# Kernel tuning notes

Measured on AMD Instinct MI355X. Metric: run time of the kernel, lower is better.

Reference implementation:

```python
import jax, jax.numpy as jnp
import numpy as np

N_NODES = 100000
N_EDGES = 1600000
D_IN = 128
D_OUT = 128
DROP_P = 0.5


def setup_inputs() -> dict:
    key = jax.random.key(0)
    k1, k2, k3, k4, k5, k6 = jax.random.split(key, 6)
    x = jax.random.normal(k1, (N_NODES, D_IN), dtype=jnp.float32)
    # xavier_normal init for w
    std = (2.0 / (D_IN + D_OUT)) ** 0.5
    w = jax.random.normal(k2, (D_IN, D_OUT), dtype=jnp.float32) * std
    b = jax.random.normal(k3, (D_OUT,), dtype=jnp.float32) * 0.01
    edge_row = jax.random.randint(k4, (N_EDGES,), 0, N_NODES, dtype=jnp.int32)
    edge_col = jax.random.randint(k5, (N_EDGES,), 0, N_NODES, dtype=jnp.int32)
    # normalized adjacency weights (e.g. 1/sqrt(d_i d_j)); use uniform positives
    edge_val = jax.random.uniform(k6, (N_EDGES,), dtype=jnp.float32)
    # dropout mask: keep with prob (1-p), scaled by 1/(1-p)
    km = jax.random.fold_in(key, 7)
    keep = jax.random.uniform(km, (N_NODES, D_IN)) >= DROP_P
    dropout_mask = keep.astype(jnp.float32) / (1.0 - DROP_P)
    return {"x": x, "w": w, "b": b, "edge_row": edge_row,
            "edge_col": edge_col, "edge_val": edge_val,
            "dropout_mask": dropout_mask}


def reference(x, w, b, edge_row, edge_col, edge_val, dropout_mask):
    # dropout (training mode) -> dense mm -> spmm(adj, xw) -> +b -> relu
    h = (x * dropout_mask) @ w                      # [N, D_OUT]
    msgs = h[edge_col] * edge_val[:, None]          # gather src feats, scale [E, D_OUT]
    agg = jax.ops.segment_sum(msgs, edge_row, num_segments=N_NODES)  # scatter-add to dst
    return jax.nn.relu(agg + b)
```

## Files before the change

### kernel.cpp

```cpp
#include <hip/hip_runtime.h>

#define N_NODES 100000
#define N_EDGES 1600000
#define D 128
#define MAXDEG 48

#define GEMM_NB ((N_NODES + 63) / 64)
#define HIST_NB (N_EDGES / 256)
#define TOTAL_NB (GEMM_NB + HIST_NB)

typedef __attribute__((ext_vector_type(8))) short short8;
typedef __attribute__((ext_vector_type(4))) short short4v;
typedef __attribute__((ext_vector_type(4))) float floatx4;
typedef __attribute__((ext_vector_type(2))) float floatx2;

__device__ __forceinline__ short f2bf(float f) {
    unsigned u = __float_as_uint(f);
    u += 0x7FFFu + ((u >> 16) & 1u);
    return (short)(u >> 16);
}

#define LDSK 136
__global__ __launch_bounds__(256) void gemm_hist_fill(const float* __restrict__ x,
                                                      const float* __restrict__ mask,
                                                      const float* __restrict__ w,
                                                      unsigned short* __restrict__ h,
                                                      const int* __restrict__ erow,
                                                      const int* __restrict__ ecol,
                                                      const float* __restrict__ eval,
                                                      int* __restrict__ deg,
                                                      unsigned long long* __restrict__ pairs) {
    const unsigned bid = blockIdx.x;
    const int t = threadIdx.x;

    if (bid % 5 != 0) {
        const int hi = (int)(bid - bid / 5 - 1);
        const int e = hi * 256 + t;
        const int r = erow[e];
        const int k = atomicAdd(&deg[r], 1);
        if (k < MAXDEG) {
            const unsigned long long pv =
                (unsigned long long)(unsigned)ecol[e] |
                ((unsigned long long)(unsigned)__float_as_uint(eval[e]) << 32);
            pairs[(size_t)r * MAXDEG + k] = pv;
        }
        return;
    }
    const int gb = (int)(bid / 5);

    __shared__ short w_s[128 * LDSK];
#pragma unroll
    for (int i = 0; i < 4; ++i) {
        const int id = t + 256 * i;
        const int n0 = (id & 31) * 4;
        const int k0 = (id >> 5) * 4;
        short tr[4][4];
#pragma unroll
        for (int r = 0; r < 4; ++r) {
            const float4 wv = *(const float4*)(w + (size_t)(k0 + r) * D + n0);
            tr[r][0] = f2bf(wv.x); tr[r][1] = f2bf(wv.y);
            tr[r][2] = f2bf(wv.z); tr[r][3] = f2bf(wv.w);
        }
#pragma unroll
        for (int c = 0; c < 4; ++c) {
            short4v v = {tr[0][c], tr[1][c], tr[2][c], tr[3][c]};
            *(short4v*)(&w_s[(n0 + c) * LDSK + k0]) = v;
        }
    }
    __syncthreads();

    const int wave = t >> 6, lane = t & 63;
    const int m = lane & 15, quad = lane >> 4;
    const int r0w = gb * 64 + wave * 16;
    int arow = r0w + m;
    if (arow >= N_NODES) arow = N_NODES - 1;
    const floatx4* xp4 = (const floatx4*)(x + (size_t)arow * D);
    const floatx4* mp4 = (const floatx4*)(mask + (size_t)arow * D);

    floatx4 acc[8];
#pragma unroll
    for (int tt = 0; tt < 8; ++tt) acc[tt] = (floatx4){0.f, 0.f, 0.f, 0.f};

#pragma unroll
    for (int kc = 0; kc < 4; ++kc) {
        const int kb = kc * 32 + quad * 8;
        const floatx4 xa = __builtin_nontemporal_load(xp4 + kb / 4);
        const floatx4 xb = __builtin_nontemporal_load(xp4 + kb / 4 + 1);
        const floatx4 ma = __builtin_nontemporal_load(mp4 + kb / 4);
        const floatx4 mb = __builtin_nontemporal_load(mp4 + kb / 4 + 1);
        short8 a;
#pragma unroll
        for (int j = 0; j < 4; ++j) a[j] = f2bf(xa[j] * ma[j]);
#pragma unroll
        for (int j = 0; j < 4; ++j) a[4 + j] = f2bf(xb[j] * mb[j]);
#pragma unroll
        for (int tt = 0; tt < 8; ++tt) {
            const short8 bfrag = *(const short8*)(&w_s[(tt * 16 + m) * LDSK + kb]);
            acc[tt] = __builtin_amdgcn_mfma_f32_16x16x32_bf16(a, bfrag, acc[tt], 0, 0, 0);
        }
    }

    __syncthreads();
    short* ep = w_s + wave * 16 * LDSK;
#pragma unroll
    for (int tt = 0; tt < 8; ++tt) {
        const int col = tt * 16 + m;
#pragma unroll
        for (int i = 0; i < 4; ++i)
            ep[(quad * 4 + i) * LDSK + col] = f2bf(acc[tt][i]);
    }
    __syncthreads();

    const int rrow = lane >> 2;
    const int chunk = lane & 3;
    const int gr = r0w + rrow;
    if (gr < N_NODES) {
        const short* src = ep + rrow * LDSK + chunk * 32;
        unsigned short* dst = h + (size_t)gr * D + chunk * 32;
#pragma unroll
        for (int j = 0; j < 4; ++j)
            *(short8*)(dst + j * 8) = *(const short8*)(src + j * 8);
    }
}

__global__ __launch_bounds__(256) void gather_kernel(const unsigned* __restrict__ h2,
                                                     const int* __restrict__ deg,
                                                     const unsigned long long* __restrict__ pairs,
                                                     const float* __restrict__ b,
                                                     float* __restrict__ out) {
    const int lane = threadIdx.x & 63;
    const int rA = blockIdx.x * 8 + (threadIdx.x >> 6) * 2;
    const int rB = rA + 1;

    int dgA = deg[rA]; if (dgA > MAXDEG) dgA = MAXDEG;
    int dgB = deg[rB]; if (dgB > MAXDEG) dgB = MAXDEG;

    const int pl = (lane < MAXDEG) ? lane : (MAXDEG - 1);
    const unsigned long long pvA = pairs[(size_t)rA * MAXDEG + pl];
    const unsigned long long pvB = pairs[(size_t)rB * MAXDEG + pl];
    const unsigned cAv = (unsigned)pvA;
    const unsigned wAv = (unsigned)(pvA >> 32);
    const unsigned cBv = (unsigned)pvB;
    const unsigned wBv = (unsigned)(pvB >> 32);

    float axA = 0.f, ayA = 0.f, axB = 0.f, ayB = 0.f;
    const int mx = (dgA > dgB) ? dgA : dgB;

    for (int b0 = 0; b0 < mx; b0 += 8) {
        unsigned uA[8], uB[8];
        float vA[8], vB[8];
#pragma unroll
        for (int jj = 0; jj < 8; ++jj) {
            const int j = b0 + jj;
            const unsigned colA = (j < dgA)
                ? (unsigned)__builtin_amdgcn_readlane((int)cAv, j) : 0u;
            vA[jj] = (j < dgA)
                ? __uint_as_float((unsigned)__builtin_amdgcn_readlane((int)wAv, j)) : 0.f;
            uA[jj] = h2[(size_t)colA * 64 + lane];
            const unsigned colB = (j < dgB)
                ? (unsigned)__builtin_amdgcn_readlane((int)cBv, j) : 0u;
            vB[jj] = (j < dgB)
                ? __uint_as_float((unsigned)__builtin_amdgcn_readlane((int)wBv, j)) : 0.f;
            uB[jj] = h2[(size_t)colB * 64 + lane];
        }
#pragma unroll
        for (int jj = 0; jj < 8; ++jj) {
            axA += __uint_as_float(uA[jj] << 16) * vA[jj];
            ayA += __uint_as_float(uA[jj] & 0xFFFF0000u) * vA[jj];
            axB += __uint_as_float(uB[jj] << 16) * vB[jj];
            ayB += __uint_as_float(uB[jj] & 0xFFFF0000u) * vB[jj];
        }
    }

    const float2 bv = ((const float2*)b)[lane];
    floatx2 oA, oB;
    oA.x = fmaxf(axA + bv.x, 0.f);
    oA.y = fmaxf(ayA + bv.y, 0.f);
    oB.x = fmaxf(axB + bv.x, 0.f);
    oB.y = fmaxf(ayB + bv.y, 0.f);
    __builtin_nontemporal_store(oA, (floatx2*)(out + (size_t)rA * D) + lane);
    __builtin_nontemporal_store(oB, (floatx2*)(out + (size_t)rB * D) + lane);
}

extern "C" void kernel_launch(void* const* d_in, const int* in_sizes, int n_in,
                              void* d_out, int out_size, void* d_ws, size_t ws_size,
                              hipStream_t stream) {
    const float* x    = (const float*)d_in[0];
    const float* w    = (const float*)d_in[1];
    const float* b    = (const float*)d_in[2];
    const int*   erow = (const int*)d_in[3];
    const int*   ecol = (const int*)d_in[4];
    const float* eval = (const float*)d_in[5];
    const float* mask = (const float*)d_in[6];
    float* out = (float*)d_out;

    char* base = (char*)d_ws;
    unsigned short* h = (unsigned short*)(base);
    int* deg          = (int*)(base + 25600000);
    unsigned long long* pairs = (unsigned long long*)(base + 26000000);

    (void)hipMemsetAsync(deg, 0, N_NODES * sizeof(int), stream);

    gemm_hist_fill<<<TOTAL_NB, 256, 0, stream>>>(x, mask, w, h, erow, ecol, eval, deg, pairs);
    gather_kernel<<<N_NODES / 8, 256, 0, stream>>>((const unsigned*)h, deg, pairs, b, out);
}
```

Measured before the change: 278.5 us.

## Amortize W staging over four GEMM tiles, write h directly, deepen gather batching

GEMM blocks now each process four 64-row tiles, so the bf16 transpose of W into LDS is paid once per four tiles, and the interleave ratio with histogram blocks changes from 1:4 to 1:16. The MFMA operands are swapped so each lane holds four consecutive output columns, which lets results go straight to global memory as short4 stores and removes the LDS epilogue and its barriers. The x and mask loads drop their nontemporal hint. In the gather kernel, sixteen rows per batch are fetched before accumulating, and the weight readlanes move into the accumulate loop, raising memory-level parallelism at the cost of more registers.

```diff
diff --git a/kernel.cpp b/kernel.cpp
--- a/kernel.cpp
+++ b/kernel.cpp
@@ -5,8 +5,10 @@
 #define D 128
 #define MAXDEG 48
 
-#define GEMM_NB ((N_NODES + 63) / 64)
+#define TILES_PER_GB 4
+#define GEMM_NB 391
 #define HIST_NB (N_EDGES / 256)
+#define RATIO 17
 #define TOTAL_NB (GEMM_NB + HIST_NB)
 
 typedef __attribute__((ext_vector_type(8))) short short8;
@@ -33,8 +35,8 @@
     const unsigned bid = blockIdx.x;
     const int t = threadIdx.x;
 
-    if (bid % 5 != 0) {
-        const int hi = (int)(bid - bid / 5 - 1);
+    if (bid % RATIO != 0) {
+        const int hi = (int)(bid - bid / RATIO - 1);
         const int e = hi * 256 + t;
         const int r = erow[e];
         const int k = atomicAdd(&deg[r], 1);
@@ -46,7 +48,7 @@
         }
         return;
     }
-    const int gb = (int)(bid / 5);
+    const int gb = (int)(bid / RATIO);
 
     __shared__ short w_s[128 * LDSK];
 #pragma unroll
@@ -71,55 +73,47 @@
 
     const int wave = t >> 6, lane = t & 63;
     const int m = lane & 15, quad = lane >> 4;
-    const int r0w = gb * 64 + wave * 16;
-    int arow = r0w + m;
-    if (arow >= N_NODES) arow = N_NODES - 1;
-    const floatx4* xp4 = (const floatx4*)(x + (size_t)arow * D);
-    const floatx4* mp4 = (const floatx4*)(mask + (size_t)arow * D);
-
-    floatx4 acc[8];
-#pragma unroll
-    for (int tt = 0; tt < 8; ++tt) acc[tt] = (floatx4){0.f, 0.f, 0.f, 0.f};
-
-#pragma unroll
-    for (int kc = 0; kc < 4; ++kc) {
-        const int kb = kc * 32 + quad * 8;
-        const floatx4 xa = __builtin_nontemporal_load(xp4 + kb / 4);
-        const floatx4 xb = __builtin_nontemporal_load(xp4 + kb / 4 + 1);
-        const floatx4 ma = __builtin_nontemporal_load(mp4 + kb / 4);
-        const floatx4 mb = __builtin_nontemporal_load(mp4 + kb / 4 + 1);
-        short8 a;
-#pragma unroll
-        for (int j = 0; j < 4; ++j) a[j] = f2bf(xa[j] * ma[j]);
-#pragma unroll
-        for (int j = 0; j < 4; ++j) a[4 + j] = f2bf(xb[j] * mb[j]);
-#pragma unroll
-        for (int tt = 0; tt < 8; ++tt) {
-            const short8 bfrag = *(const short8*)(&w_s[(tt * 16 + m) * LDSK + kb]);
-            acc[tt] = __builtin_amdgcn_mfma_f32_16x16x32_bf16(a, bfrag, acc[tt], 0, 0, 0);
-        }
-    }
-
-    __syncthreads();
-    short* ep = w_s + wave * 16 * LDSK;
-#pragma unroll
-    for (int tt = 0; tt < 8; ++tt) {
-        const int col = tt * 16 + m;
-#pragma unroll
-        for (int i = 0; i < 4; ++i)
-            ep[(quad * 4 + i) * LDSK + col] = f2bf(acc[tt][i]);
-    }
-    __syncthreads();
-
-    const int rrow = lane >> 2;
-    const int chunk = lane & 3;
-    const int gr = r0w + rrow;
-    if (gr < N_NODES) {
-        const short* src = ep + rrow * LDSK + chunk * 32;
-        unsigned short* dst = h + (size_t)gr * D + chunk * 32;
-#pragma unroll
-        for (int j = 0; j < 4; ++j)
-            *(short8*)(dst + j * 8) = *(const short8*)(src + j * 8);
+
+    for (int tile = 0; tile < TILES_PER_GB; ++tile) {
+        const int r0w = (gb * TILES_PER_GB + tile) * 64 + wave * 16;
+        if (r0w >= N_NODES) break;
+        int arow = r0w + m;
+        if (arow >= N_NODES) arow = N_NODES - 1;
+        const floatx4* xp4 = (const floatx4*)(x + (size_t)arow * D);
+        const floatx4* mp4 = (const floatx4*)(mask + (size_t)arow * D);
+
+        floatx4 acc[8];
+#pragma unroll
+        for (int tt = 0; tt < 8; ++tt) acc[tt] = (floatx4){0.f, 0.f, 0.f, 0.f};
+
+#pragma unroll
+        for (int kc = 0; kc < 4; ++kc) {
+            const int kb = kc * 32 + quad * 8;
+            const floatx4 xa = xp4[kb / 4];
+            const floatx4 xb = xp4[kb / 4 + 1];
+            const floatx4 ma = mp4[kb / 4];
+            const floatx4 mb = mp4[kb / 4 + 1];
+            short8 a;
+#pragma unroll
+            for (int j = 0; j < 4; ++j) a[j] = f2bf(xa[j] * ma[j]);
+#pragma unroll
+            for (int j = 0; j < 4; ++j) a[4 + j] = f2bf(xb[j] * mb[j]);
+#pragma unroll
+            for (int tt = 0; tt < 8; ++tt) {
+                const short8 wfrag = *(const short8*)(&w_s[(tt * 16 + m) * LDSK + kb]);
+                acc[tt] = __builtin_amdgcn_mfma_f32_16x16x32_bf16(wfrag, a, acc[tt], 0, 0, 0);
+            }
+        }
+
+        if (r0w + m < N_NODES) {
+            unsigned short* hp = h + (size_t)(r0w + m) * D + quad * 4;
+#pragma unroll
+            for (int tt = 0; tt < 8; ++tt) {
+                short4v hv = {f2bf(acc[tt][0]), f2bf(acc[tt][1]),
+                              f2bf(acc[tt][2]), f2bf(acc[tt][3])};
+                *(short4v*)(hp + tt * 16) = hv;
+            }
+        }
     }
 }
 
@@ -146,29 +140,29 @@
     float axA = 0.f, ayA = 0.f, axB = 0.f, ayB = 0.f;
     const int mx = (dgA > dgB) ? dgA : dgB;
 
-    for (int b0 = 0; b0 < mx; b0 += 8) {
-        unsigned uA[8], uB[8];
-        float vA[8], vB[8];
-#pragma unroll
-        for (int jj = 0; jj < 8; ++jj) {
+    for (int b0 = 0; b0 < mx; b0 += 16) {
+        unsigned uA[16], uB[16];
+#pragma unroll
+        for (int jj = 0; jj < 16; ++jj) {
             const int j = b0 + jj;
             const unsigned colA = (j < dgA)
                 ? (unsigned)__builtin_amdgcn_readlane((int)cAv, j) : 0u;
-            vA[jj] = (j < dgA)
-                ? __uint_as_float((unsigned)__builtin_amdgcn_readlane((int)wAv, j)) : 0.f;
             uA[jj] = h2[(size_t)colA * 64 + lane];
             const unsigned colB = (j < dgB)
                 ? (unsigned)__builtin_amdgcn_readlane((int)cBv, j) : 0u;
-            vB[jj] = (j < dgB)
+            uB[jj] = h2[(size_t)colB * 64 + lane];
+        }
+#pragma unroll
+        for (int jj = 0; jj < 16; ++jj) {
+            const int j = b0 + jj;
+            const float vA = (j < dgA)
+                ? __uint_as_float((unsigned)__builtin_amdgcn_readlane((int)wAv, j)) : 0.f;
+            const float vB = (j < dgB)
                 ? __uint_as_float((unsigned)__builtin_amdgcn_readlane((int)wBv, j)) : 0.f;
-            uB[jj] = h2[(size_t)colB * 64 + lane];
-        }
-#pragma unroll
-        for (int jj = 0; jj < 8; ++jj) {
-            axA += __uint_as_float(uA[jj] << 16) * vA[jj];
-            ayA += __uint_as_float(uA[jj] & 0xFFFF0000u) * vA[jj];
-            axB += __uint_as_float(uB[jj] << 16) * vB[jj];
-            ayB += __uint_as_float(uB[jj] & 0xFFFF0000u) * vB[jj];
+            axA += __uint_as_float(uA[jj] << 16) * vA;
+            ayA += __uint_as_float(uA[jj] & 0xFFFF0000u) * vA;
+            axB += __uint_as_float(uB[jj] << 16) * vB;
+            ayB += __uint_as_float(uB[jj] & 0xFFFF0000u) * vB;
         }
     }
 
```

Result: slower. 308.3 us (+10.7%).

## Process two 64-row tiles per GEMM block with register prefetch of inputs

Applied to the files above, without the earlier changes.

Each GEMM block now handles 128 rows in two 64-row passes. This amortizes the bf16 transpose of W into LDS over twice as many rows and halves the GEMM block count. The x and mask loads for the first tile are issued before the W staging, and the second tile's loads are issued before the first tile's epilogue, to overlap global latency with compute. It also gives the epilogue its own LDS buffer, removing the barriers, and changes the hist/GEMM block interleave ratio to 9. The cost is more registers and LDS per block, which may lower occupancy.

```diff
diff --git a/kernel.cpp b/kernel.cpp
--- a/kernel.cpp
+++ b/kernel.cpp
@@ -5,7 +5,7 @@
 #define D 128
 #define MAXDEG 48
 
-#define GEMM_NB ((N_NODES + 63) / 64)
+#define GEMM_NB 782
 #define HIST_NB (N_EDGES / 256)
 #define TOTAL_NB (GEMM_NB + HIST_NB)
 
@@ -33,8 +33,8 @@
     const unsigned bid = blockIdx.x;
     const int t = threadIdx.x;
 
-    if (bid % 5 != 0) {
-        const int hi = (int)(bid - bid / 5 - 1);
+    if (bid % 9 != 0) {
+        const int hi = (int)(bid - bid / 9 - 1);
         const int e = hi * 256 + t;
         const int r = erow[e];
         const int k = atomicAdd(&deg[r], 1);
@@ -46,9 +46,30 @@
         }
         return;
     }
-    const int gb = (int)(bid / 5);
+    const int gb = (int)(bid / 9);
+
+    const int wave = t >> 6, lane = t & 63;
+    const int m = lane & 15, quad = lane >> 4;
+    const int r0w1 = gb * 128 + wave * 16;
+    const int r0w2 = r0w1 + 64;
+    const bool t2 = (gb * 128 + 64) < N_NODES;
+
+    int arow1 = r0w1 + m;
+    if (arow1 >= N_NODES) arow1 = N_NODES - 1;
+    const floatx4* xp1 = (const floatx4*)(x + (size_t)arow1 * D);
+    const floatx4* mp1 = (const floatx4*)(mask + (size_t)arow1 * D);
+
+    floatx4 xv[8], mv[8];
+#pragma unroll
+    for (int kc = 0; kc < 4; ++kc) {
+        xv[2 * kc]     = __builtin_nontemporal_load(xp1 + kc * 8 + quad * 2);
+        xv[2 * kc + 1] = __builtin_nontemporal_load(xp1 + kc * 8 + quad * 2 + 1);
+        mv[2 * kc]     = __builtin_nontemporal_load(mp1 + kc * 8 + quad * 2);
+        mv[2 * kc + 1] = __builtin_nontemporal_load(mp1 + kc * 8 + quad * 2 + 1);
+    }
 
     __shared__ short w_s[128 * LDSK];
+    __shared__ short ep_s[64 * LDSK];
 #pragma unroll
     for (int i = 0; i < 4; ++i) {
         const int id = t + 256 * i;
@@ -69,25 +90,14 @@
     }
     __syncthreads();
 
-    const int wave = t >> 6, lane = t & 63;
-    const int m = lane & 15, quad = lane >> 4;
-    const int r0w = gb * 64 + wave * 16;
-    int arow = r0w + m;
-    if (arow >= N_NODES) arow = N_NODES - 1;
-    const floatx4* xp4 = (const floatx4*)(x + (size_t)arow * D);
-    const floatx4* mp4 = (const floatx4*)(mask + (size_t)arow * D);
-
-    floatx4 acc[8];
-#pragma unroll
-    for (int tt = 0; tt < 8; ++tt) acc[tt] = (floatx4){0.f, 0.f, 0.f, 0.f};
-
+    floatx4 acc1[8];
+#pragma unroll
+    for (int tt = 0; tt < 8; ++tt) acc1[tt] = (floatx4){0.f, 0.f, 0.f, 0.f};
 #pragma unroll
     for (int kc = 0; kc < 4; ++kc) {
         const int kb = kc * 32 + quad * 8;
-        const floatx4 xa = __builtin_nontemporal_load(xp4 + kb / 4);
-        const floatx4 xb = __builtin_nontemporal_load(xp4 + kb / 4 + 1);
-        const floatx4 ma = __builtin_nontemporal_load(mp4 + kb / 4);
-        const floatx4 mb = __builtin_nontemporal_load(mp4 + kb / 4 + 1);
+        const floatx4 xa = xv[2 * kc], xb = xv[2 * kc + 1];
+        const floatx4 ma = mv[2 * kc], mb = mv[2 * kc + 1];
         short8 a;
 #pragma unroll
         for (int j = 0; j < 4; ++j) a[j] = f2bf(xa[j] * ma[j]);
@@ -96,30 +106,84 @@
 #pragma unroll
         for (int tt = 0; tt < 8; ++tt) {
             const short8 bfrag = *(const short8*)(&w_s[(tt * 16 + m) * LDSK + kb]);
-            acc[tt] = __builtin_amdgcn_mfma_f32_16x16x32_bf16(a, bfrag, acc[tt], 0, 0, 0);
-        }
-    }
-
-    __syncthreads();
-    short* ep = w_s + wave * 16 * LDSK;
-#pragma unroll
-    for (int tt = 0; tt < 8; ++tt) {
-        const int col = tt * 16 + m;
-#pragma unroll
-        for (int i = 0; i < 4; ++i)
-            ep[(quad * 4 + i) * LDSK + col] = f2bf(acc[tt][i]);
-    }
-    __syncthreads();
-
-    const int rrow = lane >> 2;
-    const int chunk = lane & 3;
-    const int gr = r0w + rrow;
-    if (gr < N_NODES) {
-        const short* src = ep + rrow * LDSK + chunk * 32;
-        unsigned short* dst = h + (size_t)gr * D + chunk * 32;
-#pragma unroll
-        for (int j = 0; j < 4; ++j)
-            *(short8*)(dst + j * 8) = *(const short8*)(src + j * 8);
+            acc1[tt] = __builtin_amdgcn_mfma_f32_16x16x32_bf16(a, bfrag, acc1[tt], 0, 0, 0);
+        }
+    }
+
+    floatx4 xw[8], mw[8];
+    if (t2) {
+        int arow2 = r0w2 + m;
+        if (arow2 >= N_NODES) arow2 = N_NODES - 1;
+        const floatx4* xp2 = (const floatx4*)(x + (size_t)arow2 * D);
+        const floatx4* mp2 = (const floatx4*)(mask + (size_t)arow2 * D);
+#pragma unroll
+        for (int kc = 0; kc < 4; ++kc) {
+            xw[2 * kc]     = __builtin_nontemporal_load(xp2 + kc * 8 + quad * 2);
+            xw[2 * kc + 1] = __builtin_nontemporal_load(xp2 + kc * 8 + quad * 2 + 1);
+            mw[2 * kc]     = __builtin_nontemporal_load(mp2 + kc * 8 + quad * 2);
+            mw[2 * kc + 1] = __builtin_nontemporal_load(mp2 + kc * 8 + quad * 2 + 1);
+        }
+    }
+
+    short* ep = ep_s + wave * 16 * LDSK;
+    {
+#pragma unroll
+        for (int tt = 0; tt < 8; ++tt) {
+            const int col = tt * 16 + m;
+#pragma unroll
+            for (int i = 0; i < 4; ++i)
+                ep[(quad * 4 + i) * LDSK + col] = f2bf(acc1[tt][i]);
+        }
+        const int rrow = lane >> 2, chunk = lane & 3;
+        const int gr = r0w1 + rrow;
+        if (gr < N_NODES) {
+            const short* src = ep + rrow * LDSK + chunk * 32;
+            unsigned short* dst = h + (size_t)gr * D + chunk * 32;
+#pragma unroll
+            for (int j = 0; j < 4; ++j)
+                *(short8*)(dst + j * 8) = *(const short8*)(src + j * 8);
+        }
+    }
+
+    if (!t2) return;
+
+    floatx4 acc2[8];
+#pragma unroll
+    for (int tt = 0; tt < 8; ++tt) acc2[tt] = (floatx4){0.f, 0.f, 0.f, 0.f};
+#pragma unroll
+    for (int kc = 0; kc < 4; ++kc) {
+        const int kb = kc * 32 + quad * 8;
+        const floatx4 xa = xw[2 * kc], xb = xw[2 * kc + 1];
+        const floatx4 ma = mw[2 * kc], mb = mw[2 * kc + 1];
+        short8 a;
+#pragma unroll
+        for (int j = 0; j < 4; ++j) a[j] = f2bf(xa[j] * ma[j]);
+#pragma unroll
+        for (int j = 0; j < 4; ++j) a[4 + j] = f2bf(xb[j] * mb[j]);
+#pragma unroll
+        for (int tt = 0; tt < 8; ++tt) {
+            const short8 bfrag = *(const short8*)(&w_s[(tt * 16 + m) * LDSK + kb]);
+            acc2[tt] = __builtin_amdgcn_mfma_f32_16x16x32_bf16(a, bfrag, acc2[tt], 0, 0, 0);
+        }
+    }
+
+    {
+#pragma unroll
+        for (int tt = 0; tt < 8; ++tt) {
+            const int col = tt * 16 + m;
+#pragma unroll
+            for (int i = 0; i < 4; ++i)
+                ep[(quad * 4 + i) * LDSK + col] = f2bf(acc2[tt][i]);
+        }
+        const int rrow = lane >> 2, chunk = lane & 3;
+        const int gr = r0w2 + rrow;
+        if (gr < N_NODES) {
+            const short* src = ep + rrow * LDSK + chunk * 32;
+            unsigned short* dst = h + (size_t)gr * D + chunk * 32;
+#pragma unroll
+            for (int j = 0; j < 4; ++j)
+                *(short8*)(dst + j * 8) = *(const short8*)(src + j * 8);
+        }
     }
 }
 
```

Result: no change. 276.4 us (-0.8%).
